# Optimization experiments

Measured on AMD Instinct MI355X. Metric: run time of the kernel, lower is better.

Reference implementation:

```python
import jax, jax.numpy as jnp
import numpy as np

N, L, S, D, H, DK = 4, 2048, 2048, 1024, 16, 64


def setup_inputs() -> dict:
    key = jax.random.key(0)
    kq, kk, kv, kwq, kwo = jax.random.split(key, 5)
    Q = jax.random.normal(kq, (N, L, D), dtype=jnp.float32)
    K = jax.random.normal(kk, (N, S, D), dtype=jnp.float32)
    V = jax.random.normal(kv, (N, S, D), dtype=jnp.float32)
    # per-head query projection weights (the source reuses Lq for K and V too)
    Wq = jax.random.normal(kwq, (H, DK, D), dtype=jnp.float32) * (D ** -0.5)
    # output projection Lo: Linear(h*dv -> Dv), weight shape (out, in)
    Wo = jax.random.normal(kwo, (D, H * DK), dtype=jnp.float32) * ((H * DK) ** -0.5)
    return {"Q": Q, "K": K, "V": V, "Wq": Wq, "Wo": Wo}


def reference(Q, K, V, Wq, Wo):
    dk = Wq.shape[1]
    # Faithful to source: ALL of q, k, v are projected with the Lq weights.
    q = jnp.einsum('nld,hkd->hnlk', Q, Wq)   # (H,N,L,dk)
    k = jnp.einsum('nsd,hkd->hnsk', K, Wq)   # (H,N,S,dk)
    v = jnp.einsum('nsd,hkd->hnsk', V, Wq)   # (H,N,S,dk)
    scale = jnp.asarray(dk, Q.dtype) ** 0.5
    scores = jnp.einsum('hnlk,hnsk->hnls', q, k) / scale  # (H,N,L,S)
    # Faithful to F.softmax(dot) with no dim on a 3D tensor: torch picks dim=0
    # (the batch axis N); here that is axis=1 of the head-stacked (H,N,L,S).
    attn = jax.nn.softmax(scores, axis=1)
    heads = jnp.einsum('hnls,hnsk->hnlk', attn, v)        # (H,N,L,dk)
    # concat heads along last dim -> (N,L,H*dk)
    heads = jnp.transpose(heads, (1, 2, 0, 3)).reshape(Q.shape[0], Q.shape[1], -1)
    return heads @ Wo.T  # (N,L,Dv)
```

## Files before the change

### kernel.cpp

```cpp
#include <hip/hip_runtime.h>
#include <hip/hip_bf16.h>

typedef __attribute__((ext_vector_type(8))) short short8;
typedef __attribute__((ext_vector_type(4))) short short4v;
typedef __attribute__((ext_vector_type(4))) float float4v;

#define DEVI static __device__ __forceinline__

#if __has_builtin(__builtin_amdgcn_exp2f)
#define EXP2(x) __builtin_amdgcn_exp2f(x)
#else
#define EXP2(x) exp2f(x)
#endif

DEVI unsigned short f2bf(float f) {
  unsigned int u = __builtin_bit_cast(unsigned int, f);
  u += 0x7fffu + ((u >> 16) & 1u);
  return (unsigned short)(u >> 16);
}

DEVI short8 pack8(float4v a, float4v b) {
  struct P4 { __hip_bfloat162 x, y, z, w; } t;
  t.x = __float22bfloat162_rn(make_float2(a[0], a[1]));
  t.y = __float22bfloat162_rn(make_float2(a[2], a[3]));
  t.z = __float22bfloat162_rn(make_float2(b[0], b[1]));
  t.w = __float22bfloat162_rn(make_float2(b[2], b[3]));
  short8 r;
  __builtin_memcpy(&r, &t, 16);
  return r;
}

DEVI short4v pack4(float a, float b, float c, float d) {
  struct P2 { __hip_bfloat162 x, y; } t;
  t.x = __float22bfloat162_rn(make_float2(a, b));
  t.y = __float22bfloat162_rn(make_float2(c, d));
  short4v r;
  __builtin_memcpy(&r, &t, 8);
  return r;
}

DEVI void gload16(const void* src, void* lds_dst) {
  __builtin_amdgcn_global_load_lds(
      (const __attribute__((address_space(1))) void*)src,
      (__attribute__((address_space(3))) void*)lds_dst, 16, 0, 0);
}

template<int AF32, int CMODE>
__global__ __launch_bounds__(256, 2)
void gemm_bt128(const void* __restrict__ Ap, const float* __restrict__ Bp,
                void* __restrict__ Cp, int M, int Nc, int Kd, float oscale)
{
  __shared__ alignas(16) short As[2][128 * 40];
  __shared__ alignas(16) short Bs[2][128 * 40];

  const int tid = threadIdx.x;
  const int lane = tid & 63;
  const int wid = tid >> 6;
  const int rl = lane & 15;
  const int g = lane >> 4;
  const int bm = blockIdx.x * 128;
  const int bn = blockIdx.y * 128;
  const int wm = (wid >> 1) * 64;
  const int wn = (wid & 1) * 64;
  const int srow = tid >> 1;
  const int k0 = (tid & 1) * 16;

  float4v acc[4][4];
#pragma unroll
  for (int i = 0; i < 4; ++i)
#pragma unroll
    for (int j = 0; j < 4; ++j) acc[i][j] = (float4v)(0.0f);

  const float* Af = (const float*)Ap;
  const unsigned short* Ab = (const unsigned short*)Ap;

  float4v afr[4], bfr[4];
  short8 ah[2], bh[2];

  const int NK = Kd >> 5;

  auto loadA = [&](int ks) {
    size_t base = (size_t)(bm + srow) * Kd + ks * 32 + k0;
    if constexpr (AF32 != 0) {
      afr[0] = *(const float4v*)(Af + base);
      afr[1] = *(const float4v*)(Af + base + 4);
      afr[2] = *(const float4v*)(Af + base + 8);
      afr[3] = *(const float4v*)(Af + base + 12);
    } else {
      ah[0] = *(const short8*)(Ab + base);
      ah[1] = *(const short8*)(Ab + base + 8);
    }
  };
  auto loadB = [&](int ks) {
    size_t base = (size_t)(bn + srow) * Kd + ks * 32 + k0;
    bfr[0] = *(const float4v*)(Bp + base);
    bfr[1] = *(const float4v*)(Bp + base + 4);
    bfr[2] = *(const float4v*)(Bp + base + 8);
    bfr[3] = *(const float4v*)(Bp + base + 12);
  };
  auto packAB = [&]() {
    if constexpr (AF32 != 0) {
      ah[0] = pack8(afr[0], afr[1]);
      ah[1] = pack8(afr[2], afr[3]);
    }
    bh[0] = pack8(bfr[0], bfr[1]);
    bh[1] = pack8(bfr[2], bfr[3]);
  };
  auto writeLDS = [&](int b) {
    *(short8*)(As[b] + srow * 40 + k0)     = ah[0];
    *(short8*)(As[b] + srow * 40 + k0 + 8) = ah[1];
    *(short8*)(Bs[b] + srow * 40 + k0)     = bh[0];
    *(short8*)(Bs[b] + srow * 40 + k0 + 8) = bh[1];
  };

  loadA(0);
  loadB(0);
  packAB();
  writeLDS(0);
  __syncthreads();

  for (int ks = 0; ks < NK; ++ks) {
    if (ks + 1 < NK) { loadA(ks + 1); loadB(ks + 1); }

    const int b = ks & 1;
    short8 a8[4], b8[4];
#pragma unroll
    for (int mt = 0; mt < 4; ++mt)
      a8[mt] = *(const short8*)(As[b] + (wm + mt * 16 + rl) * 40 + 8 * g);
#pragma unroll
    for (int nt = 0; nt < 4; ++nt)
      b8[nt] = *(const short8*)(Bs[b] + (wn + nt * 16 + rl) * 40 + 8 * g);
#pragma unroll
    for (int mt = 0; mt < 4; ++mt)
#pragma unroll
      for (int nt = 0; nt < 4; ++nt)
        acc[mt][nt] = __builtin_amdgcn_mfma_f32_16x16x32_bf16(a8[mt], b8[nt], acc[mt][nt], 0, 0, 0);

    if (ks + 1 < NK) {
      packAB();
      writeLDS(b ^ 1);
    }
    __syncthreads();
  }

#pragma unroll
  for (int mt = 0; mt < 4; ++mt)
#pragma unroll
    for (int nt = 0; nt < 4; ++nt) {
      const int col = bn + wn + nt * 16 + rl;
      const int row0 = bm + wm + mt * 16 + 4 * g;
      if constexpr (CMODE == 1) {
        float* C = (float*)Cp;
#pragma unroll
        for (int r = 0; r < 4; ++r)
          C[(size_t)(row0 + r) * Nc + col] = acc[mt][nt][r];
      } else if constexpr (CMODE == 0) {
        unsigned short* C = (unsigned short*)Cp;
#pragma unroll
        for (int r = 0; r < 4; ++r)
          C[(size_t)(row0 + r) * Nc + col] = f2bf(acc[mt][nt][r] * oscale);
      } else {
        unsigned short* C = (unsigned short*)Cp;
        short4v w = pack4(acc[mt][nt][0], acc[mt][nt][1], acc[mt][nt][2], acc[mt][nt][3]);
        *(short4v*)(C + (size_t)col * M + row0) = w;
      }
    }
}

__global__ __launch_bounds__(512, 2)
void attn_bn(const unsigned short* __restrict__ qb,
             const unsigned short* __restrict__ kb,
             const unsigned short* __restrict__ vtb,
             unsigned short* __restrict__ hb)
{
  __shared__ alignas(128) char smem[131072];

  const int tid = threadIdx.x;
  const int lane = tid & 63;
  const int wid = tid >> 6;
  const int rl = lane & 15;
  const int g = lane >> 4;
  const int h = blockIdx.y;
  const int l0 = blockIdx.x * 128 + wid * 16;

  short8 qf[4][2];
#pragma unroll
  for (int n = 0; n < 4; ++n)
#pragma unroll
    for (int dh = 0; dh < 2; ++dh)
      qf[n][dh] = *(const short8*)(qb + (size_t)(n * 2048 + l0 + rl) * 1024 + h * 64 + dh * 32 + 8 * g);

  float4v ha[4][4];
#pragma unroll
  for (int n = 0; n < 4; ++n)
#pragma unroll
    for (int t = 0; t < 4; ++t) ha[n][t] = (float4v)(0.0f);

  const size_t koff0 = ((size_t)(wid * 2048) + (size_t)(lane >> 3)) * 1024
                     + (size_t)(h * 64) + (size_t)(((lane & 7) ^ (lane >> 3)) * 8);
  const size_t voff0 = ((size_t)(h * 64) + (size_t)(lane >> 2)) * 8192
                     + (size_t)((wid - 4) * 2048)
                     + (size_t)((((lane & 3) ^ ((lane >> 3) & 3)) * 8));

  auto stage = [&](int step, int b) {
    if (wid < 4) {
      char* kdst = smem + b * 32768 + wid * 4096;
      const unsigned short* ksrc = kb + koff0 + (size_t)step * 32 * 1024;
#pragma unroll
      for (int ii = 0; ii < 4; ++ii)
        gload16(ksrc + ii * 8192, kdst + ii * 1024);
    } else {
      char* vdst = smem + b * 32768 + 16384 + (wid - 4) * 4096;
      const unsigned short* vsrc = vtb + voff0 + (size_t)step * 32;
#pragma unroll
      for (int ii = 0; ii < 4; ++ii)
        gload16(vsrc + (size_t)ii * 16 * 8192, vdst + ii * 1024);
    }
  };

  stage(0, 0);
  stage(1, 1);
  stage(2, 2);
  asm volatile("s_waitcnt vmcnt(8)" ::: "memory");
  __builtin_amdgcn_s_barrier();

  const unsigned xr = ((unsigned)((rl >> 1) & 3)) << 4;
  const unsigned half = ((unsigned)(g & 1)) << 3;

  for (int to = 0; to < 16; ++to) {
#pragma unroll
    for (int ti = 0; ti < 4; ++ti) {
      const int t = to * 4 + ti;
      char* kbase = smem + ti * 32768;
      char* vbase = kbase + 16384;

      float4v sc[4][2];
#pragma unroll
      for (int n = 0; n < 4; ++n) {
        char* kn = kbase + n * 4096;
#pragma unroll
        for (int ss = 0; ss < 2; ++ss) {
          const int srw = ss * 16 + rl;
          const unsigned sw = ((unsigned)(srw & 7)) << 4;
          short8 kf0 = *(const short8*)(kn + srw * 128 + ((16u * (unsigned)g) ^ sw));
          short8 kf1 = *(const short8*)(kn + srw * 128 + ((64u + 16u * (unsigned)g) ^ sw));
          float4v c = (float4v)(0.0f);
          c = __builtin_amdgcn_mfma_f32_16x16x32_bf16(kf0, qf[n][0], c, 0, 0, 0);
          c = __builtin_amdgcn_mfma_f32_16x16x32_bf16(kf1, qf[n][1], c, 0, 0, 0);
          sc[n][ss] = c;
        }
      }

#pragma unroll
      for (int ss = 0; ss < 2; ++ss) {
        float ex[4][4];
#pragma unroll
        for (int n = 0; n < 4; ++n)
#pragma unroll
          for (int r = 0; r < 4; ++r)
            ex[n][r] = EXP2(fminf(sc[n][ss][r], 24.0f));
#pragma unroll
        for (int r = 0; r < 4; ++r) {
          float inv = __builtin_amdgcn_rcpf((ex[0][r] + ex[1][r]) + (ex[2][r] + ex[3][r]) + 1e-30f);
          ex[0][r] *= inv; ex[1][r] *= inv; ex[2][r] *= inv; ex[3][r] *= inv;
        }
        short4v pf[4];
#pragma unroll
        for (int n = 0; n < 4; ++n)
          pf[n] = pack4(ex[n][0], ex[n][1], ex[n][2], ex[n][3]);

        const unsigned chunk0 = 2u * (unsigned)ss + ((unsigned)g >> 1);
#pragma unroll
        for (int n = 0; n < 4; ++n) {
          char* vn = vbase + n * 4096;
#pragma unroll
          for (int t4 = 0; t4 < 4; ++t4) {
            const char* rowp = vn + (t4 * 16 + rl) * 64;
            short4v va = *(const short4v*)(rowp + (((chunk0 << 4) ^ xr) + half));
            ha[n][t4] = __builtin_amdgcn_mfma_f32_16x16x16bf16_1k(va, pf[n], ha[n][t4], 0, 0, 0);
          }
        }
      }

      if (t + 3 < 64) stage(t + 3, (ti + 3) & 3);
      asm volatile("s_waitcnt vmcnt(8)" ::: "memory");
      __builtin_amdgcn_s_barrier();
    }
  }

#pragma unroll
  for (int n = 0; n < 4; ++n)
#pragma unroll
    for (int tt = 0; tt < 4; ++tt) {
      short4v w = pack4(ha[n][tt][0], ha[n][tt][1], ha[n][tt][2], ha[n][tt][3]);
      size_t off = (size_t)(n * 2048 + l0 + rl) * 1024 + h * 64 + tt * 16 + 4 * g;
      *(short4v*)(hb + off) = w;
    }
}

extern "C" void kernel_launch(void* const* d_in, const int* in_sizes, int n_in,
                              void* d_out, int out_size, void* d_ws, size_t ws_size,
                              hipStream_t stream)
{
  const float* Q  = (const float*)d_in[0];
  const float* K  = (const float*)d_in[1];
  const float* V  = (const float*)d_in[2];
  const float* Wq = (const float*)d_in[3];
  const float* Wo = (const float*)d_in[4];

  unsigned short* qb = (unsigned short*)d_ws;
  unsigned short* kw = qb + (size_t)8192 * 1024;
  unsigned short* vt = kw + (size_t)8192 * 1024;
  unsigned short* hw = qb;

  const float CS = 0.18033688011112042f;

  dim3 gg(64, 8), bb(256);
  gemm_bt128<1, 0><<<gg, bb, 0, stream>>>(Q, Wq, qb, 8192, 1024, 1024, CS);
  gemm_bt128<1, 0><<<gg, bb, 0, stream>>>(K, Wq, kw, 8192, 1024, 1024, 1.0f);
  gemm_bt128<1, 2><<<gg, bb, 0, stream>>>(V, Wq, vt, 8192, 1024, 1024, 1.0f);
  attn_bn<<<dim3(16, 16), dim3(512), 0, stream>>>(qb, kw, vt, hw);
  gemm_bt128<0, 1><<<gg, bb, 0, stream>>>(hw, Wo, (float*)d_out, 8192, 1024, 1024, 1.0f);
}
```

Measured before the change: 273.5 us.

## Split attention batch dimension across wave pairs with LDS partial-sum exchange

The attention kernel now launches 1024 threads per block. Each of 16 waves handles half of the batch (softmax) axis for a 16-row query slice, and partial exponent sums are exchanged through an extra 32KB LDS region. K/V staging is spread across twice as many waves with half the loads each. The goal is more wave-level parallelism and lower per-wave register pressure, at the cost of an additional barrier per tile and a larger LDS footprint that limits blocks per CU.

```diff
diff --git a/kernel.cpp b/kernel.cpp
--- a/kernel.cpp
+++ b/kernel.cpp
@@ -167,13 +167,13 @@
     }
 }
 
-__global__ __launch_bounds__(512, 2)
+__global__ __launch_bounds__(1024, 4)
 void attn_bn(const unsigned short* __restrict__ qb,
              const unsigned short* __restrict__ kb,
              const unsigned short* __restrict__ vtb,
              unsigned short* __restrict__ hb)
 {
-  __shared__ alignas(128) char smem[131072];
+  __shared__ alignas(128) char smem[163840];
 
   const int tid = threadIdx.x;
   const int lane = tid & 63;
@@ -181,51 +181,58 @@
   const int rl = lane & 15;
   const int g = lane >> 4;
   const int h = blockIdx.y;
-  const int l0 = blockIdx.x * 128 + wid * 16;
-
-  short8 qf[4][2];
-#pragma unroll
-  for (int n = 0; n < 4; ++n)
+  const int rg = wid & 7;
+  const int nh = wid >> 3;
+  const int n0 = nh * 2;
+  const int l0 = blockIdx.x * 128 + rg * 16;
+
+  short8 qf[2][2];
+#pragma unroll
+  for (int j = 0; j < 2; ++j)
 #pragma unroll
     for (int dh = 0; dh < 2; ++dh)
-      qf[n][dh] = *(const short8*)(qb + (size_t)(n * 2048 + l0 + rl) * 1024 + h * 64 + dh * 32 + 8 * g);
-
-  float4v ha[4][4];
-#pragma unroll
-  for (int n = 0; n < 4; ++n)
-#pragma unroll
-    for (int t = 0; t < 4; ++t) ha[n][t] = (float4v)(0.0f);
-
-  const size_t koff0 = ((size_t)(wid * 2048) + (size_t)(lane >> 3)) * 1024
+      qf[j][dh] = *(const short8*)(qb + (size_t)((n0 + j) * 2048 + l0 + rl) * 1024 + h * 64 + dh * 32 + 8 * g);
+
+  float4v ha[2][4];
+#pragma unroll
+  for (int j = 0; j < 2; ++j)
+#pragma unroll
+    for (int t = 0; t < 4; ++t) ha[j][t] = (float4v)(0.0f);
+
+  const int kn = wid >> 1;
+  const int kh = wid & 1;
+  const size_t koff0 = ((size_t)(kn * 2048 + kh * 16) + (size_t)(lane >> 3)) * 1024
                      + (size_t)(h * 64) + (size_t)(((lane & 7) ^ (lane >> 3)) * 8);
-  const size_t voff0 = ((size_t)(h * 64) + (size_t)(lane >> 2)) * 8192
-                     + (size_t)((wid - 4) * 2048)
+  const int vn = (wid - 8) >> 1;
+  const int vh = wid & 1;
+  const size_t voff0 = ((size_t)(h * 64 + vh * 32) + (size_t)(lane >> 2)) * 8192
+                     + (size_t)(vn * 2048)
                      + (size_t)((((lane & 3) ^ ((lane >> 3) & 3)) * 8));
 
   auto stage = [&](int step, int b) {
-    if (wid < 4) {
-      char* kdst = smem + b * 32768 + wid * 4096;
+    if (wid < 8) {
+      char* kdst = smem + b * 32768 + kn * 4096 + kh * 2048;
       const unsigned short* ksrc = kb + koff0 + (size_t)step * 32 * 1024;
-#pragma unroll
-      for (int ii = 0; ii < 4; ++ii)
-        gload16(ksrc + ii * 8192, kdst + ii * 1024);
+      gload16(ksrc, kdst);
+      gload16(ksrc + 8192, kdst + 1024);
     } else {
-      char* vdst = smem + b * 32768 + 16384 + (wid - 4) * 4096;
+      char* vdst = smem + b * 32768 + 16384 + vn * 4096 + vh * 2048;
       const unsigned short* vsrc = vtb + voff0 + (size_t)step * 32;
-#pragma unroll
-      for (int ii = 0; ii < 4; ++ii)
-        gload16(vsrc + (size_t)ii * 16 * 8192, vdst + ii * 1024);
+      gload16(vsrc, vdst);
+      gload16(vsrc + (size_t)16 * 8192, vdst + 1024);
     }
   };
 
   stage(0, 0);
   stage(1, 1);
   stage(2, 2);
-  asm volatile("s_waitcnt vmcnt(8)" ::: "memory");
+  asm volatile("s_waitcnt vmcnt(4)" ::: "memory");
   __builtin_amdgcn_s_barrier();
 
   const unsigned xr = ((unsigned)((rl >> 1) & 3)) << 4;
   const unsigned half = ((unsigned)(g & 1)) << 3;
+  char* exW = smem + 131072 + rg * 2048 + nh * 1024 + lane * 16;
+  char* exR = smem + 131072 + rg * 2048 + (nh ^ 1) * 1024 + lane * 16;
 
   for (int to = 0; to < 16; ++to) {
 #pragma unroll
@@ -234,66 +241,78 @@
       char* kbase = smem + ti * 32768;
       char* vbase = kbase + 16384;
 
-      float4v sc[4][2];
-#pragma unroll
-      for (int n = 0; n < 4; ++n) {
-        char* kn = kbase + n * 4096;
+      float4v sc[2][2];
+#pragma unroll
+      for (int j = 0; j < 2; ++j) {
+        char* kn_ = kbase + (n0 + j) * 4096;
 #pragma unroll
         for (int ss = 0; ss < 2; ++ss) {
           const int srw = ss * 16 + rl;
           const unsigned sw = ((unsigned)(srw & 7)) << 4;
-          short8 kf0 = *(const short8*)(kn + srw * 128 + ((16u * (unsigned)g) ^ sw));
-          short8 kf1 = *(const short8*)(kn + srw * 128 + ((64u + 16u * (unsigned)g) ^ sw));
+          short8 kf0 = *(const short8*)(kn_ + srw * 128 + ((16u * (unsigned)g) ^ sw));
+          short8 kf1 = *(const short8*)(kn_ + srw * 128 + ((64u + 16u * (unsigned)g) ^ sw));
           float4v c = (float4v)(0.0f);
-          c = __builtin_amdgcn_mfma_f32_16x16x32_bf16(kf0, qf[n][0], c, 0, 0, 0);
-          c = __builtin_amdgcn_mfma_f32_16x16x32_bf16(kf1, qf[n][1], c, 0, 0, 0);
-          sc[n][ss] = c;
+          c = __builtin_amdgcn_mfma_f32_16x16x32_bf16(kf0, qf[j][0], c, 0, 0, 0);
+          c = __builtin_amdgcn_mfma_f32_16x16x32_bf16(kf1, qf[j][1], c, 0, 0, 0);
+          sc[j][ss] = c;
         }
       }
 
+      float ex[2][2][4];
+      float4v ps[2];
 #pragma unroll
       for (int ss = 0; ss < 2; ++ss) {
-        float ex[4][4];
-#pragma unroll
-        for (int n = 0; n < 4; ++n)
+#pragma unroll
+        for (int j = 0; j < 2; ++j)
 #pragma unroll
           for (int r = 0; r < 4; ++r)
-            ex[n][r] = EXP2(fminf(sc[n][ss][r], 24.0f));
+            ex[j][ss][r] = EXP2(fminf(sc[j][ss][r], 24.0f));
+#pragma unroll
+        for (int r = 0; r < 4; ++r)
+          ps[ss][r] = ex[0][ss][r] + ex[1][ss][r];
+        *(float4v*)(exW + ss * 16384) = ps[ss];
+      }
+      __builtin_amdgcn_s_barrier();
+
+#pragma unroll
+      for (int ss = 0; ss < 2; ++ss) {
+        float4v po = *(const float4v*)(exR + ss * 16384);
+        short4v pf[2];
 #pragma unroll
         for (int r = 0; r < 4; ++r) {
-          float inv = __builtin_amdgcn_rcpf((ex[0][r] + ex[1][r]) + (ex[2][r] + ex[3][r]) + 1e-30f);
-          ex[0][r] *= inv; ex[1][r] *= inv; ex[2][r] *= inv; ex[3][r] *= inv;
+          float inv = __builtin_amdgcn_rcpf(ps[ss][r] + po[r] + 1e-30f);
+          ex[0][ss][r] *= inv;
+          ex[1][ss][r] *= inv;
         }
-        short4v pf[4];
-#pragma unroll
-        for (int n = 0; n < 4; ++n)
-          pf[n] = pack4(ex[n][0], ex[n][1], ex[n][2], ex[n][3]);
+#pragma unroll
+        for (int j = 0; j < 2; ++j)
+          pf[j] = pack4(ex[j][ss][0], ex[j][ss][1], ex[j][ss][2], ex[j][ss][3]);
 
         const unsigned chunk0 = 2u * (unsigned)ss + ((unsigned)g >> 1);
 #pragma unroll
-        for (int n = 0; n < 4; ++n) {
-          char* vn = vbase + n * 4096;
+        for (int j = 0; j < 2; ++j) {
+          char* vn_ = vbase + (n0 + j) * 4096;
 #pragma unroll
           for (int t4 = 0; t4 < 4; ++t4) {
-            const char* rowp = vn + (t4 * 16 + rl) * 64;
+            const char* rowp = vn_ + (t4 * 16 + rl) * 64;
             short4v va = *(const short4v*)(rowp + (((chunk0 << 4) ^ xr) + half));
-            ha[n][t4] = __builtin_amdgcn_mfma_f32_16x16x16bf16_1k(va, pf[n], ha[n][t4], 0, 0, 0);
+            ha[j][t4] = __builtin_amdgcn_mfma_f32_16x16x16bf16_1k(va, pf[j], ha[j][t4], 0, 0, 0);
           }
         }
       }
 
       if (t + 3 < 64) stage(t + 3, (ti + 3) & 3);
-      asm volatile("s_waitcnt vmcnt(8)" ::: "memory");
+      asm volatile("s_waitcnt vmcnt(4)" ::: "memory");
       __builtin_amdgcn_s_barrier();
     }
   }
 
 #pragma unroll
-  for (int n = 0; n < 4; ++n)
+  for (int j = 0; j < 2; ++j)
 #pragma unroll
     for (int tt = 0; tt < 4; ++tt) {
-      short4v w = pack4(ha[n][tt][0], ha[n][tt][1], ha[n][tt][2], ha[n][tt][3]);
-      size_t off = (size_t)(n * 2048 + l0 + rl) * 1024 + h * 64 + tt * 16 + 4 * g;
+      short4v w = pack4(ha[j][tt][0], ha[j][tt][1], ha[j][tt][2], ha[j][tt][3]);
+      size_t off = (size_t)((n0 + j) * 2048 + l0 + rl) * 1024 + h * 64 + tt * 16 + 4 * g;
       *(short4v*)(hb + off) = w;
     }
 }
@@ -319,6 +338,6 @@
   gemm_bt128<1, 0><<<gg, bb, 0, stream>>>(Q, Wq, qb, 8192, 1024, 1024, CS);
   gemm_bt128<1, 0><<<gg, bb, 0, stream>>>(K, Wq, kw, 8192, 1024, 1024, 1.0f);
   gemm_bt128<1, 2><<<gg, bb, 0, stream>>>(V, Wq, vt, 8192, 1024, 1024, 1.0f);
-  attn_bn<<<dim3(16, 16), dim3(512), 0, stream>>>(qb, kw, vt, hw);
+  attn_bn<<<dim3(16, 16), dim3(1024), 0, stream>>>(qb, kw, vt, hw);
   gemm_bt128<0, 1><<<gg, bb, 0, stream>>>(hw, Wo, (float*)d_out, 8192, 1024, 1024, 1.0f);
 }
```

Measured after the change: 280.6 us. 2.6% more time.

## Use 16x16x32 MFMA for PV with permuted V-transpose layout

Applied to the files above, without the earlier changes.

Replaces the pair of 16x16x16 bf16 MFMAs per PV tile with a single 16x16x32 MFMA. It does this by permuting the row order in which the projection GEMM writes the transposed V, so that each lane's 8 contiguous bf16 values match the K-slot ordering of the packed probabilities from both score halves. This halves the PV MFMA instruction count and turns two 8-byte LDS reads into one 16-byte read. In exchange it raises register pressure, since both halves of the exp values stay live at once, and it depends on the layout permutation being consistent between producer and consumer.

```diff
diff --git a/kernel.cpp b/kernel.cpp
--- a/kernel.cpp
+++ b/kernel.cpp
@@ -162,7 +162,9 @@
       } else {
         unsigned short* C = (unsigned short*)Cp;
         short4v w = pack4(acc[mt][nt][0], acc[mt][nt][1], acc[mt][nt][2], acc[mt][nt][3]);
-        *(short4v*)(C + (size_t)col * M + row0) = w;
+        const int u = row0 & 31;
+        const int pm = (row0 & ~31) | (((u >> 2) & 3) << 3) | (((u >> 4) & 1) << 2);
+        *(short4v*)(C + (size_t)col * M + pm) = w;
       }
     }
 }
@@ -224,8 +226,7 @@
   asm volatile("s_waitcnt vmcnt(8)" ::: "memory");
   __builtin_amdgcn_s_barrier();
 
-  const unsigned xr = ((unsigned)((rl >> 1) & 3)) << 4;
-  const unsigned half = ((unsigned)(g & 1)) << 3;
+  const unsigned voffr = ((unsigned)(g ^ ((rl >> 1) & 3))) << 4;
 
   for (int to = 0; to < 16; ++to) {
 #pragma unroll
@@ -251,34 +252,37 @@
         }
       }
 
+      float ex[4][2][4];
 #pragma unroll
       for (int ss = 0; ss < 2; ++ss) {
-        float ex[4][4];
 #pragma unroll
         for (int n = 0; n < 4; ++n)
 #pragma unroll
           for (int r = 0; r < 4; ++r)
-            ex[n][r] = EXP2(fminf(sc[n][ss][r], 24.0f));
+            ex[n][ss][r] = EXP2(fminf(sc[n][ss][r], 24.0f));
 #pragma unroll
         for (int r = 0; r < 4; ++r) {
-          float inv = __builtin_amdgcn_rcpf((ex[0][r] + ex[1][r]) + (ex[2][r] + ex[3][r]) + 1e-30f);
-          ex[0][r] *= inv; ex[1][r] *= inv; ex[2][r] *= inv; ex[3][r] *= inv;
+          float inv = __builtin_amdgcn_rcpf((ex[0][ss][r] + ex[1][ss][r])
+                                          + (ex[2][ss][r] + ex[3][ss][r]) + 1e-30f);
+          ex[0][ss][r] *= inv; ex[1][ss][r] *= inv;
+          ex[2][ss][r] *= inv; ex[3][ss][r] *= inv;
         }
-        short4v pf[4];
-#pragma unroll
-        for (int n = 0; n < 4; ++n)
-          pf[n] = pack4(ex[n][0], ex[n][1], ex[n][2], ex[n][3]);
-
-        const unsigned chunk0 = 2u * (unsigned)ss + ((unsigned)g >> 1);
-#pragma unroll
-        for (int n = 0; n < 4; ++n) {
-          char* vn = vbase + n * 4096;
-#pragma unroll
-          for (int t4 = 0; t4 < 4; ++t4) {
-            const char* rowp = vn + (t4 * 16 + rl) * 64;
-            short4v va = *(const short4v*)(rowp + (((chunk0 << 4) ^ xr) + half));
-            ha[n][t4] = __builtin_amdgcn_mfma_f32_16x16x16bf16_1k(va, pf[n], ha[n][t4], 0, 0, 0);
-          }
+      }
+      short8 pf8[4];
+#pragma unroll
+      for (int n = 0; n < 4; ++n) {
+        float4v e0 = {ex[n][0][0], ex[n][0][1], ex[n][0][2], ex[n][0][3]};
+        float4v e1 = {ex[n][1][0], ex[n][1][1], ex[n][1][2], ex[n][1][3]};
+        pf8[n] = pack8(e0, e1);
+      }
+
+#pragma unroll
+      for (int n = 0; n < 4; ++n) {
+        char* vn = vbase + n * 4096;
+#pragma unroll
+        for (int t4 = 0; t4 < 4; ++t4) {
+          short8 va = *(const short8*)(vn + (t4 * 16 + rl) * 64 + voffr);
+          ha[n][t4] = __builtin_amdgcn_mfma_f32_16x16x32_bf16(va, pf8[n], ha[n][t4], 0, 0, 0);
         }
       }
 
```

New measurement: 260.7 us. 1.05x faster.
